# Kernel optimization log

Hardware: AMD Instinct MI355X
Metric: run time of the kernel (lower is better)

Reference implementation:

```python
import jax, jax.numpy as jnp
import numpy as np

T, B, H, V = 256, 16, 512, 32000


def setup_inputs() -> dict:
    key = jax.random.key(0)
    k0, k1, k2, k3, k4, k5 = jax.random.split(key, 6)
    inp = jax.random.randint(k0, (T, B), 0, V)
    emb = jax.random.normal(k1, (V, H), dtype=jnp.float32) * 0.02
    w1 = jax.random.normal(k2, (H, 2 * H), dtype=jnp.float32) * (1.0 / np.sqrt(2 * H))
    b1 = jnp.zeros((H,), dtype=jnp.float32)
    dec_w = jax.random.normal(k3, (V, H), dtype=jnp.float32) * (1.0 / np.sqrt(H))
    dec_b = jnp.zeros((V,), dtype=jnp.float32)
    return {"input": inp, "batch_size": B, "emb": emb, "w1": w1, "b1": b1,
            "dec_w": dec_w, "dec_b": dec_b}


def reference(input, batch_size, emb, w1, b1, dec_w, dec_b):
    # encoder: embedding lookup -> [T, B, H]
    x = emb[input]
    h0 = jnp.zeros((batch_size, emb.shape[1]), dtype=emb.dtype)
    # w1 acts on concat([x_t, h]); split into input / recurrent halves
    wx, wh = w1[:, :H], w1[:, H:]

    def step(h, xt):
        h_new = jnp.tanh(xt @ wx.T + h @ wh.T + b1)  # [B, H]
        return h_new, h_new

    h_last, outputs = jax.lax.scan(step, h0, x)  # outputs: [T, B, H]
    logits = outputs @ dec_w.T + dec_b  # [T, B, V]
    decode = logits.reshape(-1, logits.shape[-1])  # [T*B, V]
    return decode, h_last
```

## Files before the change

### kernel.cpp

```cpp
#include <hip/hip_runtime.h>
#include <hip/hip_bf16.h>

#define T_STEPS 256
#define BATCH   16
#define HID     512
#define VOCAB   32000
#define M_TOT   (T_STEPS * BATCH)
#define KT_DEC  16
#define NT2     125
#define NTILES  (16 * NT2)

typedef __attribute__((ext_vector_type(8))) short s8v;
typedef __attribute__((ext_vector_type(4))) float f4v;
typedef __attribute__((ext_vector_type(16))) float f16v;
typedef unsigned short ushort_t;
typedef unsigned long long u64;

__device__ __forceinline__ unsigned short f2bf_rne(float f) {
  unsigned u = __float_as_uint(f);
  unsigned r = u + 0x7fffu + ((u >> 16) & 1u);
  return (unsigned short)(r >> 16);
}
__device__ __forceinline__ float bf2f(unsigned short s) {
  return __uint_as_float(((unsigned)s) << 16);
}
__device__ __forceinline__ int unit_swz(int r, int kg) {
  return r * 4 + (kg ^ ((r >> 1) & 3));
}
__device__ __forceinline__ void gload16(const void* g, void* l) {
  __builtin_amdgcn_global_load_lds(
      (const __attribute__((address_space(1))) unsigned int*)g,
      (__attribute__((address_space(3))) unsigned int*)l, 16, 0, 0);
}
#define MFMA16(a, b, c) __builtin_amdgcn_mfma_f32_16x16x32_bf16((a), (b), (c), 0, 0, 0)
#define MFMA32(a, b, c) __builtin_amdgcn_mfma_f32_32x32x16_bf16((a), (b), (c), 0, 0, 0)
#define AGENT_LD(p) __hip_atomic_load((p), __ATOMIC_RELAXED, __HIP_MEMORY_SCOPE_AGENT)
#define AGENT_ST(p, v) __hip_atomic_store((p), (v), __ATOMIC_RELAXED, __HIP_MEMORY_SCOPE_AGENT)
#define SCHED0() __builtin_amdgcn_sched_barrier(0)

__global__ __launch_bounds__(256, 2) void head_kernel(
    const int* __restrict__ tok, const float* __restrict__ emb,
    const float* __restrict__ w1, const float* __restrict__ b1f,
    float* __restrict__ pre,
    const float* __restrict__ dec_w, ushort_t* __restrict__ bhi,
    ushort_t* __restrict__ blo, int do_split) {
  if (blockIdx.x >= 128) {
    if (!do_split) return;
    const int pid = blockIdx.x - 128;
    const int nt = pid >> 4, ks = pid & 15;
    const int tid = threadIdx.x;
#pragma unroll
    for (int h = 0; h < 2; ++h) {
      int us = h * 256 + tid;
      int r = us >> 2, kg = us & 3;
      const float* src = dec_w + (size_t)(nt * 128 + r) * HID + ks * 32 + kg * 8;
      float4 v0 = *(const float4*)src;
      float4 v1 = *(const float4*)(src + 4);
      float av[8] = {v0.x, v0.y, v0.z, v0.w, v1.x, v1.y, v1.z, v1.w};
      s8v hi, lo;
#pragma unroll
      for (int j = 0; j < 8; ++j) {
        unsigned short hh = f2bf_rne(av[j]);
        hi[j] = (short)hh;
        lo[j] = (short)f2bf_rne(av[j] - bf2f(hh));
      }
      size_t base = ((size_t)(nt * 16 + ks) * 512 + unit_swz(r, kg)) * 8;
      *(s8v*)(bhi + base) = hi;
      *(s8v*)(blo + base) = lo;
    }
    return;
  }
  __shared__ s8v Ah[512], Al[512], Bh[512], Bl[512];
  const int mt = blockIdx.x & 31, nt = blockIdx.x >> 5;
  const int tid = threadIdx.x;
  const int lane = tid & 63, wave = tid >> 6;
  const int wm = wave >> 1, wn = wave & 1;
  const int m0 = mt * 128, n0 = nt * 128;
  f4v acc[4][4] = {};

  for (int ks = 0; ks < 16; ++ks) {
    const int k0 = ks * 32;
#pragma unroll
    for (int c = 0; c < 2; ++c) {
      int idx = c * 256 + tid;
      int r = idx >> 2, kg = idx & 3;
      int kgp = kg ^ (r & 3);
      int t_ = tok[m0 + r];
      const float* as = emb + (size_t)t_ * HID + k0 + kg * 8;
      float4 a0 = *(const float4*)as;
      float4 a1 = *(const float4*)(as + 4);
      float av[8] = {a0.x, a0.y, a0.z, a0.w, a1.x, a1.y, a1.z, a1.w};
      s8v ah, al;
#pragma unroll
      for (int j = 0; j < 8; ++j) {
        unsigned short h = f2bf_rne(av[j]);
        ah[j] = (short)h;
        al[j] = (short)f2bf_rne(av[j] - bf2f(h));
      }
      Ah[r * 4 + kgp] = ah;  Al[r * 4 + kgp] = al;
      const float* bs = w1 + (size_t)(n0 + r) * 1024 + k0 + kg * 8;
      float4 b0 = *(const float4*)bs;
      float4 b1v = *(const float4*)(bs + 4);
      float bv[8] = {b0.x, b0.y, b0.z, b0.w, b1v.x, b1v.y, b1v.z, b1v.w};
      s8v bh, bl;
#pragma unroll
      for (int j = 0; j < 8; ++j) {
        unsigned short h = f2bf_rne(bv[j]);
        bh[j] = (short)h;
        bl[j] = (short)f2bf_rne(bv[j] - bf2f(h));
      }
      Bh[r * 4 + kgp] = bh;  Bl[r * 4 + kgp] = bl;
    }
    __syncthreads();
    s8v afh[4], afl[4], bfh[4], bfl[4];
#pragma unroll
    for (int f = 0; f < 4; ++f) {
      int rA = wm * 64 + f * 16 + (lane & 15);
      afh[f] = Ah[rA * 4 + ((lane >> 4) ^ (rA & 3))];
      afl[f] = Al[rA * 4 + ((lane >> 4) ^ (rA & 3))];
      int rB = wn * 64 + f * 16 + (lane & 15);
      bfh[f] = Bh[rB * 4 + ((lane >> 4) ^ (rB & 3))];
      bfl[f] = Bl[rB * 4 + ((lane >> 4) ^ (rB & 3))];
    }
#pragma unroll
    for (int i = 0; i < 4; ++i)
#pragma unroll
      for (int j = 0; j < 4; ++j)
        acc[i][j] = MFMA16(afh[i], bfh[j], acc[i][j]);
#pragma unroll
    for (int i = 0; i < 4; ++i)
#pragma unroll
      for (int j = 0; j < 4; ++j)
        acc[i][j] = MFMA16(afl[i], bfh[j], acc[i][j]);
#pragma unroll
    for (int i = 0; i < 4; ++i)
#pragma unroll
      for (int j = 0; j < 4; ++j)
        acc[i][j] = MFMA16(afh[i], bfl[j], acc[i][j]);
    __syncthreads();
  }
#pragma unroll
  for (int j = 0; j < 4; ++j) {
    int col = n0 + wn * 64 + j * 16 + (lane & 15);
    float bias = b1f[col];
#pragma unroll
    for (int i = 0; i < 4; ++i)
#pragma unroll
      for (int rg = 0; rg < 4; ++rg) {
        int row = m0 + wm * 64 + i * 16 + (lane >> 4) * 4 + rg;
        pre[(size_t)row * HID + col] = acc[i][j][rg] + bias;
      }
  }
}

__global__ __launch_bounds__(512, 2) void scanodec_kernel(
    const float* __restrict__ w1, const float* __restrict__ pre,
    u64* hbuf, ushort_t* o_hi, ushort_t* o_lo, int* wq, int* scnt,
    const ushort_t* __restrict__ bhi, const ushort_t* __restrict__ blo,
    const float* __restrict__ dec_b, float* __restrict__ out,
    float* __restrict__ h_last_out, int ntiles) {
  extern __shared__ char LB[];
  const int tid = threadIdx.x;

  if (blockIdx.x < 128) {
    float* wLds  = (float*)LB;
    float* hsb   = (float*)(LB + 65536);
    float* partb = (float*)(LB + 69632);
    const int bp = blockIdx.x & 7;
    const int sg = blockIdx.x >> 3;
    const int b0 = bp * 2, b1i = b0 + 1;

#pragma unroll
    for (int k = 0; k < 8; ++k) {
      int uid = k * 512 + tid;
      int r = uid >> 7, u = uid & 127;
      float4 v = *(const float4*)(w1 + (size_t)(sg * 32 + r) * 1024 + 512 + u * 4);
      int dst = r * 512 + (u >> 3) * 32 + (((u & 7) ^ (r & 7)) << 2);
      *(float4*)(&wLds[dst]) = v;
    }
    __syncthreads();

    const int i = tid & 31, s = tid >> 5;
    const int rowbase = i * 512 + s * 32;
    const int isw = i & 7;
    unsigned* oh32 = (unsigned*)o_hi;
    unsigned* ol32 = (unsigned*)o_lo;

    for (int t = 0; t < T_STEPS; ++t) {
      const int cur = t & 1, nxt = cur ^ 1;

      float pv = 0.f;
      if (tid < 64) {
        int bl = tid >> 5, ii = tid & 31;
        pv = pre[(size_t)(t * BATCH + b0 + bl) * HID + sg * 32 + ii];
      }

      u64* p0 = hbuf + ((size_t)cur * BATCH + b0) * HID + tid;
      u64* p1 = hbuf + ((size_t)cur * BATCH + b1i) * HID + tid;
      u64 e0 = AGENT_LD(p0);
      u64 e1 = AGENT_LD(p1);
      int spins = 0;
      while ((unsigned)(e0 >> 32) != (unsigned)t || (unsigned)(e1 >> 32) != (unsigned)t) {
        __builtin_amdgcn_s_sleep(1);
        if ((unsigned)(e0 >> 32) != (unsigned)t) e0 = AGENT_LD(p0);
        if ((unsigned)(e1 >> 32) != (unsigned)t) e1 = AGENT_LD(p1);
        if (++spins > (1 << 21)) break;
      }
      hsb[tid] = __uint_as_float((unsigned)e0);
      hsb[512 + tid] = __uint_as_float((unsigned)e1);
      __syncthreads();

      float a0 = 0.f, a1 = 0.f;
#pragma unroll
      for (int u = 0; u < 8; ++u) {
        float4 w = *(const float4*)(&wLds[rowbase + ((u ^ isw) << 2)]);
        float4 h0 = *(const float4*)(&hsb[s * 32 + (u << 2)]);
        float4 h1 = *(const float4*)(&hsb[512 + s * 32 + (u << 2)]);
        a0 += w.x * h0.x + w.y * h0.y + w.z * h0.z + w.w * h0.w;
        a1 += w.x * h1.x + w.y * h1.y + w.z * h1.z + w.w * h1.w;
      }
      partb[s * 33 + i] = a0;
      partb[528 + s * 33 + i] = a1;
      __syncthreads();

      if (tid < 64) {
        int bl = tid >> 5, ii = tid & 31;
        float ssum = 0.f;
#pragma unroll
        for (int ss = 0; ss < 16; ++ss) ssum += partb[bl * 528 + ss * 33 + ii];
        ssum += pv;
        float hn = tanhf(ssum);
        int b = b0 + bl;
        u64 ev = ((u64)(unsigned)(t + 1) << 32) | (u64)__float_as_uint(hn);
        AGENT_ST(hbuf + ((size_t)nxt * BATCH + b) * HID + sg * 32 + ii, ev);
        int m = t * BATCH + b;
        int mt = m >> 7, r = m & 127;
        int kg = ii >> 3, e = ii & 7;
        unsigned hi_u = f2bf_rne(hn);
        unsigned lo_u = f2bf_rne(hn - bf2f((unsigned short)hi_u));
        unsigned hi_n = __shfl_down(hi_u, 1);
        unsigned lo_n = __shfl_down(lo_u, 1);
        if ((ii & 1) == 0) {
          size_t u32i = ((size_t)(mt * 16 + sg) * 512 + unit_swz(r, kg)) * 4 + (e >> 1);
          AGENT_ST(oh32 + u32i, hi_u | (hi_n << 16));
          AGENT_ST(ol32 + u32i, lo_u | (lo_n << 16));
        }
        if (t == T_STEPS - 1) h_last_out[(size_t)b * HID + sg * 32 + ii] = hn;
      }
      if ((t & 15) == 15) {
        __syncthreads();
        if (tid == 0)
          __hip_atomic_fetch_add(scnt + (t >> 4) * 16, 1,
                                 __ATOMIC_RELEASE, __HIP_MEMORY_SCOPE_AGENT);
      }
    }
    __syncthreads();
  }

  {
    s8v* SB = (s8v*)LB;
    int* slot = (int*)(LB + 131072);
    const int lane = tid & 63, wv = tid >> 6;
    const int wm = wv >> 2, wn = wv & 3;
    const int lane32 = lane & 31, kh = lane >> 5;
    const int tB = wn >> 1;

    const ushort_t* gsrc;
    if (wv < 4) gsrc = (wv < 2) ? o_hi : o_lo;
    else        gsrc = (wv < 6) ? bhi : blo;

    int uB_[2][2], uA_[4][2];
#pragma unroll
    for (int tn = 0; tn < 2; ++tn)
#pragma unroll
      for (int s = 0; s < 2; ++s)
        uB_[tn][s] = (4 + tB) * 512 +
                     unit_swz((wn & 1) * 64 + tn * 32 + lane32, s * 2 + kh);
#pragma unroll
    for (int tm = 0; tm < 4; ++tm)
#pragma unroll
      for (int s = 0; s < 2; ++s)
        uA_[tm][s] = wm * 512 + unit_swz(tm * 32 + lane32, s * 2 + kh);

    for (;;) {
      if (tid == 0)
        *slot = __hip_atomic_fetch_add(wq, 1, __ATOMIC_RELAXED,
                                       __HIP_MEMORY_SCOPE_AGENT);
      __syncthreads();
      const int idx = *slot;
      if (idx >= ntiles) break;
      const int mt2 = idx / NT2, nt2 = idx % NT2;
      if (tid == 0) {
        int spins = 0;
        while (__hip_atomic_load(scnt + mt2 * 16, __ATOMIC_ACQUIRE,
                                 __HIP_MEMORY_SCOPE_AGENT) < 128) {
          __builtin_amdgcn_s_sleep(2);
          if (++spins > (1 << 22)) break;
        }
      }
      __syncthreads();

      const int gtile = ((wv < 4) ? mt2 * 2 : nt2 * 2) + (wv & 1);
      f16v acc[4][2] = {};

      {
        const char* g0 = (const char*)(gsrc + (size_t)(gtile * 16 + 0) * 4096);
        const char* g1 = (const char*)(gsrc + (size_t)(gtile * 16 + 1) * 4096);
        char* l0 = (char*)SB + wv * 8192;
        char* l1 = (char*)SB + 65536 + wv * 8192;
#pragma unroll
        for (int p = 0; p < 8; ++p) gload16(g0 + p * 1024 + (size_t)lane * 16, l0 + p * 1024);
#pragma unroll
        for (int p = 0; p < 8; ++p) gload16(g1 + p * 1024 + (size_t)lane * 16, l1 + p * 1024);
        asm volatile("s_waitcnt vmcnt(8)" ::: "memory");
        SCHED0();
        __builtin_amdgcn_s_barrier();
        SCHED0();
      }

      for (int kt = 0; kt < KT_DEC; ++kt) {
        const int c = kt & 1;
        const s8v* B0 = SB + c * 4096;

        s8v bh[2][2], bl[2][2], ah[4][2], al[4][2];
#pragma unroll
        for (int tn = 0; tn < 2; ++tn)
#pragma unroll
          for (int s = 0; s < 2; ++s) {
            bh[tn][s] = B0[uB_[tn][s]];
            bl[tn][s] = B0[1024 + uB_[tn][s]];
          }
#pragma unroll
        for (int tm = 0; tm < 2; ++tm)
#pragma unroll
          for (int s = 0; s < 2; ++s) {
            ah[tm][s] = B0[uA_[tm][s]];
            al[tm][s] = B0[1024 + uA_[tm][s]];
          }
        SCHED0();
#pragma unroll
        for (int tm = 2; tm < 4; ++tm)
#pragma unroll
          for (int s = 0; s < 2; ++s) {
            ah[tm][s] = B0[uA_[tm][s]];
            al[tm][s] = B0[1024 + uA_[tm][s]];
          }
        asm volatile("s_waitcnt lgkmcnt(8)" ::: "memory");
        SCHED0();

        __builtin_amdgcn_s_setprio(1);
#pragma unroll
        for (int s = 0; s < 2; ++s)
#pragma unroll
          for (int tn = 0; tn < 2; ++tn) {
            acc[0][tn] = MFMA32(ah[0][s], bh[tn][s], acc[0][tn]);
            acc[1][tn] = MFMA32(ah[1][s], bh[tn][s], acc[1][tn]);
          }
#pragma unroll
        for (int s = 0; s < 2; ++s)
#pragma unroll
          for (int tn = 0; tn < 2; ++tn) {
            acc[0][tn] = MFMA32(al[0][s], bh[tn][s], acc[0][tn]);
            acc[1][tn] = MFMA32(al[1][s], bh[tn][s], acc[1][tn]);
          }
#pragma unroll
        for (int s = 0; s < 2; ++s)
#pragma unroll
          for (int tn = 0; tn < 2; ++tn) {
            acc[0][tn] = MFMA32(ah[0][s], bl[tn][s], acc[0][tn]);
            acc[1][tn] = MFMA32(ah[1][s], bl[tn][s], acc[1][tn]);
          }
        __builtin_amdgcn_s_setprio(0);

        asm volatile("s_waitcnt lgkmcnt(0)" ::: "memory");
        SCHED0();
        __builtin_amdgcn_s_barrier();
        SCHED0();
        if (kt + 2 < KT_DEC) {
          const char* g = (const char*)(gsrc + (size_t)(gtile * 16 + kt + 2) * 4096);
          char* l = (char*)SB + c * 65536 + wv * 8192;
#pragma unroll
          for (int p = 0; p < 8; ++p) gload16(g + p * 1024 + (size_t)lane * 16, l + p * 1024);
        }
        SCHED0();

        __builtin_amdgcn_s_setprio(1);
#pragma unroll
        for (int s = 0; s < 2; ++s)
#pragma unroll
          for (int tn = 0; tn < 2; ++tn) {
            acc[2][tn] = MFMA32(ah[2][s], bh[tn][s], acc[2][tn]);
            acc[3][tn] = MFMA32(ah[3][s], bh[tn][s], acc[3][tn]);
          }
#pragma unroll
        for (int s = 0; s < 2; ++s)
#pragma unroll
          for (int tn = 0; tn < 2; ++tn) {
            acc[2][tn] = MFMA32(al[2][s], bh[tn][s], acc[2][tn]);
            acc[3][tn] = MFMA32(al[3][s], bh[tn][s], acc[3][tn]);
          }
#pragma unroll
        for (int s = 0; s < 2; ++s)
#pragma unroll
          for (int tn = 0; tn < 2; ++tn) {
            acc[2][tn] = MFMA32(ah[2][s], bl[tn][s], acc[2][tn]);
            acc[3][tn] = MFMA32(ah[3][s], bl[tn][s], acc[3][tn]);
          }
        __builtin_amdgcn_s_setprio(0);

        if (kt + 2 < KT_DEC) {
          asm volatile("s_waitcnt vmcnt(8)" ::: "memory");
        } else {
          asm volatile("s_waitcnt vmcnt(0)" ::: "memory");
        }
        SCHED0();
        __builtin_amdgcn_s_barrier();
        SCHED0();
      }

      const int m0 = mt2 * 256, n0 = nt2 * 256;
#pragma unroll
      for (int tn = 0; tn < 2; ++tn) {
        int col = n0 + wn * 64 + tn * 32 + lane32;
        float bias = dec_b[col];
#pragma unroll
        for (int tm = 0; tm < 4; ++tm) {
          int rowb = m0 + wm * 128 + tm * 32 + 4 * kh;
#pragma unroll
          for (int reg = 0; reg < 16; ++reg) {
            int row = rowb + (reg & 3) + 8 * (reg >> 2);
            __builtin_nontemporal_store(acc[tm][tn][reg] + bias,
                                        &out[(size_t)row * VOCAB + col]);
          }
        }
      }
      asm volatile("s_waitcnt vmcnt(0)" ::: "memory");
      SCHED0();
    }
  }
}

__global__ __launch_bounds__(256, 2) void dec_gemm_fb(
    const ushort_t* __restrict__ o_hi, const ushort_t* __restrict__ o_lo,
    const float* __restrict__ dec_w, const float* __restrict__ dec_b,
    float* __restrict__ out) {
  __shared__ s8v Ah[512], Al[512], Bh[512], Bl[512];
  const int mt = blockIdx.x, nt = blockIdx.y;
  const int tid = threadIdx.x;
  const int lane = tid & 63, wave = tid >> 6;
  const int wm = wave >> 1, wn = wave & 1;
  const int kgl = lane >> 4, lr = lane & 15;
  const int m0 = mt * 128, n0 = nt * 128;
  f4v acc[4][4] = {};

  for (int ks = 0; ks < KT_DEC; ++ks) {
    const int k0 = ks * 32;
#pragma unroll
    for (int c = 0; c < 2; ++c) {
      int idx = c * 256 + tid;
      size_t abase = (size_t)(mt * 16 + ks) * 4096 + (size_t)idx * 8;
      Ah[idx] = *(const s8v*)(o_hi + abase);
      Al[idx] = *(const s8v*)(o_lo + abase);
      int r = idx >> 2, kg = idx & 3;
      const float* bs = dec_w + (size_t)(n0 + r) * HID + k0 + kg * 8;
      float4 b0 = *(const float4*)bs;
      float4 b1v = *(const float4*)(bs + 4);
      float bv[8] = {b0.x, b0.y, b0.z, b0.w, b1v.x, b1v.y, b1v.z, b1v.w};
      s8v bh, bl;
#pragma unroll
      for (int j = 0; j < 8; ++j) {
        unsigned short h = f2bf_rne(bv[j]);
        bh[j] = (short)h;
        bl[j] = (short)f2bf_rne(bv[j] - bf2f(h));
      }
      int ub = unit_swz(r, kg);
      Bh[ub] = bh;  Bl[ub] = bl;
    }
    __syncthreads();
    s8v afh[4], afl[4], bfh[4], bfl[4];
#pragma unroll
    for (int f = 0; f < 4; ++f) {
      int rA = wm * 64 + f * 16 + lr;
      int uA = unit_swz(rA, kgl);
      afh[f] = Ah[uA];  afl[f] = Al[uA];
      int rB = wn * 64 + f * 16 + lr;
      int uB = unit_swz(rB, kgl);
      bfh[f] = Bh[uB];  bfl[f] = Bl[uB];
    }
#pragma unroll
    for (int i = 0; i < 4; ++i)
#pragma unroll
      for (int j = 0; j < 4; ++j)
        acc[i][j] = MFMA16(afh[i], bfh[j], acc[i][j]);
#pragma unroll
    for (int i = 0; i < 4; ++i)
#pragma unroll
      for (int j = 0; j < 4; ++j)
        acc[i][j] = MFMA16(afl[i], bfh[j], acc[i][j]);
#pragma unroll
    for (int i = 0; i < 4; ++i)
#pragma unroll
      for (int j = 0; j < 4; ++j)
        acc[i][j] = MFMA16(afh[i], bfl[j], acc[i][j]);
    __syncthreads();
  }
#pragma unroll
  for (int j = 0; j < 4; ++j) {
    int col = n0 + wn * 64 + j * 16 + lr;
    float bias = dec_b[col];
#pragma unroll
    for (int i = 0; i < 4; ++i)
#pragma unroll
      for (int rg = 0; rg < 4; ++rg) {
        int row = m0 + wm * 64 + i * 16 + (lane >> 4) * 4 + rg;
        __builtin_nontemporal_store(acc[i][j][rg] + bias,
                                    &out[(size_t)row * VOCAB + col]);
      }
  }
}

extern "C" void kernel_launch(void* const* d_in, const int* in_sizes, int n_in,
                              void* d_out, int out_size, void* d_ws, size_t ws_size,
                              hipStream_t stream) {
  (void)in_sizes; (void)n_in; (void)out_size;
  const int*   tok   = (const int*)d_in[0];
  const float* emb   = (const float*)d_in[2];
  const float* w1    = (const float*)d_in[3];
  const float* b1    = (const float*)d_in[4];
  const float* dec_w = (const float*)d_in[5];
  const float* dec_b = (const float*)d_in[6];
  char* ws = (char*)d_ws;
  u64*      hbuf = (u64*)(ws);
  int*      wq   = (int*)(ws + 131072);
  int*      scnt = (int*)(ws + 131136);
  ushort_t* o_hi = (ushort_t*)(ws + (2u << 20));
  ushort_t* o_lo = (ushort_t*)(ws + (6u << 20));
  float*    pre  = (float*)(ws + (18u << 20));
  ushort_t* bhi  = (ushort_t*)(ws + (26u << 20));
  ushort_t* blo  = (ushort_t*)(ws + (58u << 20));
  float* out = (float*)d_out;

  const int big = (ws_size >= (size_t)92 * 1024 * 1024) ? 1 : 0;

  hipMemsetAsync(ws, 0, 132160, stream);
  head_kernel<<<dim3(4128), dim3(256), 0, stream>>>(
      tok, emb, w1, b1, pre, dec_w, bhi, blo, big);
  hipFuncSetAttribute((const void*)scanodec_kernel,
                      hipFuncAttributeMaxDynamicSharedMemorySize, 131328);
  scanodec_kernel<<<dim3(256), dim3(512), 131328, stream>>>(
      w1, pre, hbuf, o_hi, o_lo, wq, scnt, bhi, blo, dec_b, out,
      out + (size_t)M_TOT * VOCAB, big ? NTILES : 0);
  if (!big)
    dec_gemm_fb<<<dim3(32, 250), dim3(256), 0, stream>>>(o_hi, o_lo, dec_w, dec_b, out);
}
```

Before: 678.6 us.

## Halve scan blocks by processing four batch rows per block

The recurrent scan now uses 64 blocks, each handling 4 batch rows instead of 2 across 16 hidden slices. Each block reuses its LDS-resident weight slice for twice as many batch rows. This frees 64 more blocks for the concurrent decoder GEMM and cuts the number of participants in the per-step spin synchronisation. In exchange each scan block does twice the work per step, which lengthens the serial critical path of the recurrence.

Result: slower. 1.412 ms (+108.1%).

```diff
diff --git a/kernel.cpp b/kernel.cpp
--- a/kernel.cpp
+++ b/kernel.cpp
@@ -9,6 +9,8 @@
 #define KT_DEC  16
 #define NT2     125
 #define NTILES  (16 * NT2)
+#define NSCAN   64
+#define GB      4
 
 typedef __attribute__((ext_vector_type(8))) short s8v;
 typedef __attribute__((ext_vector_type(4))) float f4v;
@@ -162,13 +164,13 @@
   extern __shared__ char LB[];
   const int tid = threadIdx.x;
 
-  if (blockIdx.x < 128) {
+  if (blockIdx.x < NSCAN) {
     float* wLds  = (float*)LB;
     float* hsb   = (float*)(LB + 65536);
-    float* partb = (float*)(LB + 69632);
-    const int bp = blockIdx.x & 7;
-    const int sg = blockIdx.x >> 3;
-    const int b0 = bp * 2, b1i = b0 + 1;
+    float* partb = (float*)(LB + 65536 + 8192);
+    const int bq = blockIdx.x & 3;
+    const int sg = blockIdx.x >> 2;
+    const int b0 = bq * GB;
 
 #pragma unroll
     for (int k = 0; k < 8; ++k) {
@@ -190,40 +192,57 @@
       const int cur = t & 1, nxt = cur ^ 1;
 
       float pv = 0.f;
-      if (tid < 64) {
+      if (tid < 32 * GB) {
         int bl = tid >> 5, ii = tid & 31;
         pv = pre[(size_t)(t * BATCH + b0 + bl) * HID + sg * 32 + ii];
       }
 
-      u64* p0 = hbuf + ((size_t)cur * BATCH + b0) * HID + tid;
-      u64* p1 = hbuf + ((size_t)cur * BATCH + b1i) * HID + tid;
-      u64 e0 = AGENT_LD(p0);
-      u64 e1 = AGENT_LD(p1);
-      int spins = 0;
-      while ((unsigned)(e0 >> 32) != (unsigned)t || (unsigned)(e1 >> 32) != (unsigned)t) {
-        __builtin_amdgcn_s_sleep(1);
-        if ((unsigned)(e0 >> 32) != (unsigned)t) e0 = AGENT_LD(p0);
-        if ((unsigned)(e1 >> 32) != (unsigned)t) e1 = AGENT_LD(p1);
-        if (++spins > (1 << 21)) break;
-      }
-      hsb[tid] = __uint_as_float((unsigned)e0);
-      hsb[512 + tid] = __uint_as_float((unsigned)e1);
+      u64 e0, e1, e2, e3;
+      {
+        u64* p0 = hbuf + ((size_t)cur * BATCH + b0 + 0) * HID + tid;
+        u64* p1 = hbuf + ((size_t)cur * BATCH + b0 + 1) * HID + tid;
+        u64* p2 = hbuf + ((size_t)cur * BATCH + b0 + 2) * HID + tid;
+        u64* p3 = hbuf + ((size_t)cur * BATCH + b0 + 3) * HID + tid;
+        e0 = AGENT_LD(p0); e1 = AGENT_LD(p1);
+        e2 = AGENT_LD(p2); e3 = AGENT_LD(p3);
+        const unsigned tg = (unsigned)t;
+        int spins = 0;
+        while ((unsigned)(e0 >> 32) != tg || (unsigned)(e1 >> 32) != tg ||
+               (unsigned)(e2 >> 32) != tg || (unsigned)(e3 >> 32) != tg) {
+          __builtin_amdgcn_s_sleep(1);
+          if ((unsigned)(e0 >> 32) != tg) e0 = AGENT_LD(p0);
+          if ((unsigned)(e1 >> 32) != tg) e1 = AGENT_LD(p1);
+          if ((unsigned)(e2 >> 32) != tg) e2 = AGENT_LD(p2);
+          if ((unsigned)(e3 >> 32) != tg) e3 = AGENT_LD(p3);
+          if (++spins > (1 << 21)) break;
+        }
+      }
+      hsb[tid]        = __uint_as_float((unsigned)e0);
+      hsb[512 + tid]  = __uint_as_float((unsigned)e1);
+      hsb[1024 + tid] = __uint_as_float((unsigned)e2);
+      hsb[1536 + tid] = __uint_as_float((unsigned)e3);
       __syncthreads();
 
-      float a0 = 0.f, a1 = 0.f;
+      float a0 = 0.f, a1 = 0.f, a2 = 0.f, a3 = 0.f;
 #pragma unroll
       for (int u = 0; u < 8; ++u) {
         float4 w = *(const float4*)(&wLds[rowbase + ((u ^ isw) << 2)]);
         float4 h0 = *(const float4*)(&hsb[s * 32 + (u << 2)]);
         float4 h1 = *(const float4*)(&hsb[512 + s * 32 + (u << 2)]);
+        float4 h2 = *(const float4*)(&hsb[1024 + s * 32 + (u << 2)]);
+        float4 h3 = *(const float4*)(&hsb[1536 + s * 32 + (u << 2)]);
         a0 += w.x * h0.x + w.y * h0.y + w.z * h0.z + w.w * h0.w;
         a1 += w.x * h1.x + w.y * h1.y + w.z * h1.z + w.w * h1.w;
-      }
-      partb[s * 33 + i] = a0;
-      partb[528 + s * 33 + i] = a1;
+        a2 += w.x * h2.x + w.y * h2.y + w.z * h2.z + w.w * h2.w;
+        a3 += w.x * h3.x + w.y * h3.y + w.z * h3.z + w.w * h3.w;
+      }
+      partb[s * 33 + i]        = a0;
+      partb[528 + s * 33 + i]  = a1;
+      partb[1056 + s * 33 + i] = a2;
+      partb[1584 + s * 33 + i] = a3;
       __syncthreads();
 
-      if (tid < 64) {
+      if (tid < 32 * GB) {
         int bl = tid >> 5, ii = tid & 31;
         float ssum = 0.f;
 #pragma unroll
@@ -293,7 +312,7 @@
       if (tid == 0) {
         int spins = 0;
         while (__hip_atomic_load(scnt + mt2 * 16, __ATOMIC_ACQUIRE,
-                                 __HIP_MEMORY_SCOPE_AGENT) < 128) {
+                                 __HIP_MEMORY_SCOPE_AGENT) < NSCAN) {
           __builtin_amdgcn_s_sleep(2);
           if (++spins > (1 << 22)) break;
         }
```
